# Performance work log

Measured on AMD Instinct MI355X. Metric: run time of the kernel, lower is better.

## Reference

```python
import jax, jax.numpy as jnp
import numpy as np


def setup_inputs() -> dict:
    key = jax.random.key(0)
    B, H, S, D = 4, 16, 2048, 128  # batch, kv heads, seq_len, head_dim
    kv_cache = jax.random.normal(key, (B, H, S, D), dtype=jnp.float32)
    return {"kv_cache": kv_cache, "rank": 64}


def reference(kv_cache, rank):
    # compress(): batched reduced SVD, truncate to `rank` components.
    orig_shape = kv_cache.shape
    S_len, D = orig_shape[-2], orig_shape[-1]
    x = kv_cache.reshape(-1, S_len, D)                 # [N, S, D]
    U, s, Vh = jnp.linalg.svd(x, full_matrices=False)  # U:[N,S,D], s:[N,D], Vh:[N,D,D]
    U_t = U[:, :, :rank]                               # [N, S, r]
    s_t = s[:, :rank]                                  # [N, r]
    Vh_t = Vh[:, :rank, :]                             # [N, r, D]
    left = U_t * s_t[:, None, :]                       # [N, S, r]  (= U * diag(s))
    # decompress(): left @ right^T, right = V[:, :, :rank] so right^T = Vh_t
    reconstructed = jnp.matmul(left, Vh_t)             # [N, S, D]
    return reconstructed.reshape(orig_shape)
```

## Files before the change

kernel.cpp:

```cpp
#include <hip/hip_runtime.h>


#define NM 64
#define SEQ 2048
#define DD 128
#define RR 64
#define NSWEEP 6
#define NROUND (NSWEEP * 64)

#define OFF_VFULL (4194304ULL)
#define OFF_NORM  (8388608ULL)
#define OFF_VT    (33554432ULL)

__device__ __forceinline__ float dot4(float4 a, float4 b) {
  return a.x * b.x + a.y * b.y + a.z * b.z + a.w * b.w;
}

template <int CTRL>
__device__ __forceinline__ float dpp_add(float x) {
  int y = __builtin_amdgcn_update_dpp(0, __float_as_int(x), CTRL, 0xf, 0xf, true);
  return x + __int_as_float(y);
}
__device__ __forceinline__ float red8(float x) {
  x = dpp_add<0xB1>(x);
  x = dpp_add<0x4E>(x);
  x = dpp_add<0x141>(x);
  return x;
}

__device__ __forceinline__ void jrot(float app, float apq, float aqq,
                                     float& c, float& s, float& tv) {
  bool ok = apq * apq > 1e-9f * app * aqq;
  float ap = ok ? apq : 1.f;
  float tau = (aqq - app) / (2.f * ap);
  float t = 1.f / (fabsf(tau) + sqrtf(1.f + tau * tau));
  t = tau < 0.f ? -t : t;
  float cc = 1.f / sqrtf(1.f + t * t);
  float ss = t * cc;
  c = ok ? cc : 1.f;
  s = ok ? ss : 0.f;
  tv = ok ? t : 0.f;
}

__device__ __forceinline__ void rot4(float c, float s, float4 p, float4 q,
                                     float4& np, float4& nq) {
  np.x = c * p.x - s * q.x;  nq.x = s * p.x + c * q.x;
  np.y = c * p.y - s * q.y;  nq.y = s * p.y + c * q.y;
  np.z = c * p.z - s * q.z;  nq.z = s * p.z + c * q.z;
  np.w = c * p.w - s * q.w;  nq.w = s * p.w + c * q.w;
}

__global__ __launch_bounds__(256) void gram_k(const float* __restrict__ X,
                                              float* __restrict__ G) {
  const int m = blockIdx.y;
  const int r0 = blockIdx.x * 32;
  const int tid = threadIdx.x;
  __shared__ __align__(16) float Xs[64][128];
  const float* Xm = X + (size_t)m * SEQ * DD;
  const int ti = tid >> 5;
  const int tj = tid & 31;
  float acc[4][4];
#pragma unroll
  for (int a = 0; a < 4; ++a)
#pragma unroll
    for (int b = 0; b < 4; ++b) acc[a][b] = 0.f;

  for (int s0 = 0; s0 < SEQ; s0 += 64) {
    __syncthreads();
    for (int t = tid; t < 2048; t += 256) {
      int s = t >> 5, c4 = t & 31;
      *(float4*)&Xs[s][c4 * 4] =
          *(const float4*)&Xm[(size_t)(s0 + s) * DD + c4 * 4];
    }
    __syncthreads();
#pragma unroll 4
    for (int s = 0; s < 64; ++s) {
      float4 av = *(const float4*)&Xs[s][r0 + 4 * ti];
      float4 bv = *(const float4*)&Xs[s][4 * tj];
      acc[0][0] += av.x * bv.x; acc[0][1] += av.x * bv.y;
      acc[0][2] += av.x * bv.z; acc[0][3] += av.x * bv.w;
      acc[1][0] += av.y * bv.x; acc[1][1] += av.y * bv.y;
      acc[1][2] += av.y * bv.z; acc[1][3] += av.y * bv.w;
      acc[2][0] += av.z * bv.x; acc[2][1] += av.z * bv.y;
      acc[2][2] += av.z * bv.z; acc[2][3] += av.z * bv.w;
      acc[3][0] += av.w * bv.x; acc[3][1] += av.w * bv.y;
      acc[3][2] += av.w * bv.z; acc[3][3] += av.w * bv.w;
    }
  }
  float* Gm = G + (size_t)m * DD * DD;
#pragma unroll
  for (int a = 0; a < 4; ++a) {
    float4 v = make_float4(acc[a][0], acc[a][1], acc[a][2], acc[a][3]);
    *(float4*)&Gm[(size_t)(r0 + 4 * ti + a) * DD + 4 * tj] = v;
  }
}

__global__ __launch_bounds__(512) void jacobi_nc_k(const float* __restrict__ G,
                                                   float* __restrict__ Vfull,
                                                   float* __restrict__ normg) {
  const int m = blockIdx.x;
  const int tid = threadIdx.x;
  const int g = tid >> 3;
  const int l = tid & 7;
  __shared__ __align__(16) float4 xch[RR * 32];
  __shared__ float nrm[RR];

  const float4* Gm4 = (const float4*)(G + (size_t)m * DD * DD);
  float4 ce[4], co[4];
#pragma unroll
  for (int j = 0; j < 4; ++j) {
    ce[j] = Gm4[(size_t)(2 * g) * 32 + l + 8 * j];
    co[j] = Gm4[(size_t)(2 * g + 1) * 32 + l + 8 * j];
  }
  float nce = 0.f, nco = 0.f;
#pragma unroll
  for (int j = 0; j < 4; ++j) {
    nce += dot4(ce[j], ce[j]);
    nco += dot4(co[j], co[j]);
  }
  nce = red8(nce);
  nco = red8(nco);

  const bool hasR = (g < 63);
  const bool hasL = (g > 0);
  float4* hE = &xch[g * 32];
  float4* hR = &xch[(g + 1) * 32];

  for (int round = 0; round < NROUND; ++round) {
    {
      float apq = 0.f;
#pragma unroll
      for (int j = 0; j < 4; ++j) apq += dot4(ce[j], co[j]);
      apq = red8(apq);
      float c, s, tv;
      jrot(nce, apq, nco, c, s, tv);
#pragma unroll
      for (int j = 0; j < 4; ++j) {
        float4 np, nq;
        rot4(c, s, ce[j], co[j], np, nq);
        ce[j] = nq; co[j] = np;
      }
      float t = nce;
      nce = nco + tv * apq;
      nco = t - tv * apq;
    }
    if (hasL) {
#pragma unroll
      for (int j = 0; j < 4; ++j) hE[l + 8 * j] = ce[j];
      if (l == 0) nrm[g] = nce;
    }
    __syncthreads();
    if (hasR) {
      float4 r4[4];
#pragma unroll
      for (int j = 0; j < 4; ++j) r4[j] = hR[l + 8 * j];
      float nr = nrm[g + 1];
      float apq = 0.f;
#pragma unroll
      for (int j = 0; j < 4; ++j) apq += dot4(co[j], r4[j]);
      apq = red8(apq);
      float c, s, tv;
      jrot(nco, apq, nr, c, s, tv);
#pragma unroll
      for (int j = 0; j < 4; ++j) {
        float4 np, nq;
        rot4(c, s, co[j], r4[j], np, nq);
        hR[l + 8 * j] = np;
        co[j] = nq;
      }
      if (l == 0) nrm[g + 1] = nco - tv * apq;
      nco = nr + tv * apq;
    }
    __syncthreads();
    if (hasL) {
#pragma unroll
      for (int j = 0; j < 4; ++j) ce[j] = hE[l + 8 * j];
      nce = nrm[g];
    }
  }

  float ne = 0.f, no_ = 0.f;
#pragma unroll
  for (int j = 0; j < 4; ++j) {
    ne += dot4(ce[j], ce[j]);
    no_ += dot4(co[j], co[j]);
  }
  ne = red8(ne);
  no_ = red8(no_);
  float4* Ve = (float4*)(Vfull + ((size_t)m * DD + 2 * g) * DD);
  float4* Vo = (float4*)(Vfull + ((size_t)m * DD + 2 * g + 1) * DD);
#pragma unroll
  for (int j = 0; j < 4; ++j) {
    Ve[l + 8 * j] = ce[j];
    Vo[l + 8 * j] = co[j];
  }
  if (l == 0) {
    normg[m * DD + 2 * g] = ne;
    normg[m * DD + 2 * g + 1] = no_;
  }
}

__global__ __launch_bounds__(128) void select_k(const float* __restrict__ Vfull,
                                                const float* __restrict__ normg,
                                                float* __restrict__ Vt) {
  const int m = blockIdx.x;
  const int t = threadIdx.x;
  __shared__ float n[DD];
  __shared__ int inv[RR];
  __shared__ float scl[RR];
  n[t] = normg[m * DD + t];
  __syncthreads();
  float nt = n[t];
  int rk = 0;
  for (int k = 0; k < DD; ++k) {
    float nk = n[k];
    rk += ((nk > nt) || (nk == nt && k < t)) ? 1 : 0;
  }
  if (rk < RR) { inv[rk] = t; scl[rk] = 1.f / sqrtf(nt); }
  __syncthreads();
  for (int r = 0; r < RR; ++r) {
    Vt[((size_t)m * RR + r) * DD + t] =
        Vfull[((size_t)m * DD + inv[r]) * DD + t] * scl[r];
  }
}

__global__ __launch_bounds__(256) void gemm1_k(const float* __restrict__ X,
                                               const float* __restrict__ Vt,
                                               float* __restrict__ W) {
  const int m = blockIdx.y;
  const int s0 = blockIdx.x * 32;
  const int tid = threadIdx.x;
  __shared__ __align__(16) float VtT[128 * 68];
  __shared__ __align__(16) float Xs[32 * 132];
  const float* Vm = Vt + (size_t)m * RR * DD;
  for (int t = tid; t < RR * DD; t += 256) {
    int r = t >> 7, c = t & 127;
    VtT[c * 68 + r] = Vm[t];
  }
  const float* Xm = X + ((size_t)m * SEQ + s0) * DD;
  for (int t = tid; t < 1024; t += 256) {
    int s = t >> 5, c4 = t & 31;
    *(float4*)&Xs[s * 132 + 4 * c4] = *(const float4*)&Xm[(size_t)s * DD + 4 * c4];
  }
  __syncthreads();
  const int ti = tid >> 4;
  const int tj = tid & 15;
  float acc[2][4] = {{0.f, 0.f, 0.f, 0.f}, {0.f, 0.f, 0.f, 0.f}};
#pragma unroll 4
  for (int k = 0; k < DD; ++k) {
    float a0 = Xs[(2 * ti) * 132 + k];
    float a1 = Xs[(2 * ti + 1) * 132 + k];
    float4 bv = *(float4*)&VtT[k * 68 + 4 * tj];
    acc[0][0] += a0 * bv.x; acc[0][1] += a0 * bv.y;
    acc[0][2] += a0 * bv.z; acc[0][3] += a0 * bv.w;
    acc[1][0] += a1 * bv.x; acc[1][1] += a1 * bv.y;
    acc[1][2] += a1 * bv.z; acc[1][3] += a1 * bv.w;
  }
  float* Wm = W + ((size_t)m * SEQ + s0) * RR;
#pragma unroll
  for (int d = 0; d < 2; ++d) {
    float4 v = make_float4(acc[d][0], acc[d][1], acc[d][2], acc[d][3]);
    *(float4*)&Wm[(size_t)(2 * ti + d) * RR + 4 * tj] = v;
  }
}

__global__ __launch_bounds__(256) void gemm2_k(const float* __restrict__ W,
                                               const float* __restrict__ Vt,
                                               float* __restrict__ out) {
  const int m = blockIdx.y;
  const int s0 = blockIdx.x * 32;
  const int tid = threadIdx.x;
  __shared__ __align__(16) float Vts[64 * 132];
  __shared__ __align__(16) float Ws[32 * 68];
  const float* Vm = Vt + (size_t)m * RR * DD;
  for (int t = tid; t < 2048; t += 256) {
    int r = t >> 5, c4 = t & 31;
    *(float4*)&Vts[r * 132 + 4 * c4] = *(const float4*)&Vm[(size_t)r * DD + 4 * c4];
  }
  const float* Wm = W + ((size_t)m * SEQ + s0) * RR;
  for (int t = tid; t < 512; t += 256) {
    int s = t >> 4, c4 = t & 15;
    *(float4*)&Ws[s * 68 + 4 * c4] = *(const float4*)&Wm[(size_t)s * RR + 4 * c4];
  }
  __syncthreads();
  const int ti = tid >> 5;
  const int tj = tid & 31;
  float acc[4][4] = {{0.f,0.f,0.f,0.f},{0.f,0.f,0.f,0.f},
                     {0.f,0.f,0.f,0.f},{0.f,0.f,0.f,0.f}};
#pragma unroll 4
  for (int k = 0; k < RR; ++k) {
    float4 bv = *(float4*)&Vts[k * 132 + 4 * tj];
    float a0 = Ws[(4 * ti + 0) * 68 + k];
    float a1 = Ws[(4 * ti + 1) * 68 + k];
    float a2 = Ws[(4 * ti + 2) * 68 + k];
    float a3 = Ws[(4 * ti + 3) * 68 + k];
    acc[0][0] += a0 * bv.x; acc[0][1] += a0 * bv.y;
    acc[0][2] += a0 * bv.z; acc[0][3] += a0 * bv.w;
    acc[1][0] += a1 * bv.x; acc[1][1] += a1 * bv.y;
    acc[1][2] += a1 * bv.z; acc[1][3] += a1 * bv.w;
    acc[2][0] += a2 * bv.x; acc[2][1] += a2 * bv.y;
    acc[2][2] += a2 * bv.z; acc[2][3] += a2 * bv.w;
    acc[3][0] += a3 * bv.x; acc[3][1] += a3 * bv.y;
    acc[3][2] += a3 * bv.z; acc[3][3] += a3 * bv.w;
  }
  float* Om = out + ((size_t)m * SEQ + s0) * DD;
#pragma unroll
  for (int d = 0; d < 4; ++d) {
    float4 v = make_float4(acc[d][0], acc[d][1], acc[d][2], acc[d][3]);
    *(float4*)&Om[(size_t)(4 * ti + d) * DD + 4 * tj] = v;
  }
}

extern "C" void kernel_launch(void* const* d_in, const int* in_sizes, int n_in,
                              void* d_out, int out_size, void* d_ws, size_t ws_size,
                              hipStream_t stream) {
  (void)in_sizes; (void)n_in; (void)out_size; (void)ws_size;
  const float* X = (const float*)d_in[0];
  float* out = (float*)d_out;
  char* ws = (char*)d_ws;
  float* G = (float*)ws;
  float* Vfull = (float*)(ws + OFF_VFULL);
  float* normg = (float*)(ws + OFF_NORM);
  float* Vt = (float*)(ws + OFF_VT);
  float* W = (float*)ws;

  gram_k<<<dim3(4, NM), 256, 0, stream>>>(X, G);
  jacobi_nc_k<<<NM, 512, 0, stream>>>(G, Vfull, normg);
  select_k<<<NM, 128, 0, stream>>>(Vfull, normg, Vt);
  gemm1_k<<<dim3(SEQ / 32, NM), 256, 0, stream>>>(X, Vt, W);
  gemm2_k<<<dim3(SEQ / 32, NM), 256, 0, stream>>>(W, Vt, out);
}
```

Baseline: 909.5 us.

## Restructure Jacobi kernel to four columns per 16-lane group with double-buffered exchange

The one-sided Jacobi kernel now has each 16-lane group hold four columns instead of two. This halves the number of groups and the per-column work per lane. The exchange now goes through a double-buffered shared array, which cuts each round from two barriers to one. Norms are recomputed at the end of every sweep, and the sweep count rises from 6 to 7, which adds rotation work in exchange for accuracy.

```diff
diff --git a/kernel.cpp b/kernel.cpp
--- a/kernel.cpp
+++ b/kernel.cpp
@@ -5,8 +5,7 @@
 #define SEQ 2048
 #define DD 128
 #define RR 64
-#define NSWEEP 6
-#define NROUND (NSWEEP * 64)
+#define NSWEEP 7
 
 #define OFF_VFULL (4194304ULL)
 #define OFF_NORM  (8388608ULL)
@@ -21,10 +20,11 @@
   int y = __builtin_amdgcn_update_dpp(0, __float_as_int(x), CTRL, 0xf, 0xf, true);
   return x + __int_as_float(y);
 }
-__device__ __forceinline__ float red8(float x) {
+__device__ __forceinline__ float red16(float x) {
   x = dpp_add<0xB1>(x);
   x = dpp_add<0x4E>(x);
   x = dpp_add<0x141>(x);
+  x = dpp_add<0x140>(x);
   return x;
 }
 
@@ -48,6 +48,27 @@
   np.y = c * p.y - s * q.y;  nq.y = s * p.y + c * q.y;
   np.z = c * p.z - s * q.z;  nq.z = s * p.z + c * q.z;
   np.w = c * p.w - s * q.w;  nq.w = s * p.w + c * q.w;
+}
+__device__ __forceinline__ float4 np4(float c, float s, float4 p, float4 q) {
+  return make_float4(c * p.x - s * q.x, c * p.y - s * q.y,
+                     c * p.z - s * q.z, c * p.w - s * q.w);
+}
+__device__ __forceinline__ float4 nq4(float c, float s, float4 p, float4 q) {
+  return make_float4(s * p.x + c * q.x, s * p.y + c * q.y,
+                     s * p.z + c * q.z, s * p.w + c * q.w);
+}
+
+__device__ __forceinline__ void rot2pair(float4* P, float4* Q,
+                                         float& npn, float& nqn) {
+  float apq = red16(dot4(P[0], Q[0]) + dot4(P[1], Q[1]));
+  float c, s, tv;
+  jrot(npn, apq, nqn, c, s, tv);
+  float4 a, b;
+  rot4(c, s, P[0], Q[0], a, b); P[0] = b; Q[0] = a;
+  rot4(c, s, P[1], Q[1], a, b); P[1] = b; Q[1] = a;
+  float t = npn;
+  npn = nqn + tv * apq;
+  nqn = t - tv * apq;
 }
 
 __global__ __launch_bounds__(256) void gram_k(const float* __restrict__ X,
@@ -95,108 +116,102 @@
   }
 }
 
-__global__ __launch_bounds__(512) void jacobi_nc_k(const float* __restrict__ G,
-                                                   float* __restrict__ Vfull,
-                                                   float* __restrict__ normg) {
+__global__ __launch_bounds__(512) void jacobi1b_k(const float* __restrict__ G,
+                                                  float* __restrict__ Vfull,
+                                                  float* __restrict__ normg) {
   const int m = blockIdx.x;
   const int tid = threadIdx.x;
-  const int g = tid >> 3;
-  const int l = tid & 7;
-  __shared__ __align__(16) float4 xch[RR * 32];
-  __shared__ float nrm[RR];
+  const int g = tid >> 4;
+  const int l = tid & 15;
+  __shared__ __align__(16) float4 xch[2][2][32][32];
 
   const float4* Gm4 = (const float4*)(G + (size_t)m * DD * DD);
-  float4 ce[4], co[4];
-#pragma unroll
-  for (int j = 0; j < 4; ++j) {
-    ce[j] = Gm4[(size_t)(2 * g) * 32 + l + 8 * j];
-    co[j] = Gm4[(size_t)(2 * g + 1) * 32 + l + 8 * j];
-  }
-  float nce = 0.f, nco = 0.f;
-#pragma unroll
-  for (int j = 0; j < 4; ++j) {
-    nce += dot4(ce[j], ce[j]);
-    nco += dot4(co[j], co[j]);
-  }
-  nce = red8(nce);
-  nco = red8(nco);
-
-  const bool hasR = (g < 63);
+  float4 c0[2], c1[2], c2[2], c3[2];
+#pragma unroll
+  for (int j = 0; j < 2; ++j) {
+    c0[j] = Gm4[(size_t)(4 * g + 0) * 32 + l + 16 * j];
+    c1[j] = Gm4[(size_t)(4 * g + 1) * 32 + l + 16 * j];
+    c2[j] = Gm4[(size_t)(4 * g + 2) * 32 + l + 16 * j];
+    c3[j] = Gm4[(size_t)(4 * g + 3) * 32 + l + 16 * j];
+  }
+  float n0 = red16(dot4(c0[0], c0[0]) + dot4(c0[1], c0[1]));
+  float n1 = red16(dot4(c1[0], c1[0]) + dot4(c1[1], c1[1]));
+  float n2 = red16(dot4(c2[0], c2[0]) + dot4(c2[1], c2[1]));
+  float n3 = red16(dot4(c3[0], c3[0]) + dot4(c3[1], c3[1]));
+
+  const bool hasR = (g < 31);
   const bool hasL = (g > 0);
-  float4* hE = &xch[g * 32];
-  float4* hR = &xch[(g + 1) * 32];
-
-  for (int round = 0; round < NROUND; ++round) {
-    {
-      float apq = 0.f;
-#pragma unroll
-      for (int j = 0; j < 4; ++j) apq += dot4(ce[j], co[j]);
-      apq = red8(apq);
-      float c, s, tv;
-      jrot(nce, apq, nco, c, s, tv);
-#pragma unroll
-      for (int j = 0; j < 4; ++j) {
-        float4 np, nq;
-        rot4(c, s, ce[j], co[j], np, nq);
-        ce[j] = nq; co[j] = np;
-      }
-      float t = nce;
-      nce = nco + tv * apq;
-      nco = t - tv * apq;
+
+  for (int sweep = 0; sweep < NSWEEP; ++sweep) {
+#pragma unroll 1
+    for (int round = 0; round < 64; ++round) {
+      const int b = round & 1;
+      float* nb = (float*)&xch[b][0][0][0];
+      rot2pair(c0, c1, n0, n1);
+      rot2pair(c2, c3, n2, n3);
+      if (hasL) {
+        xch[b][0][g][l] = c0[0];
+        xch[b][0][g][l + 16] = c0[1];
+        if (l == 0) nb[g] = n0;
+      }
+      if (hasR) {
+        xch[b][1][g][l] = c3[0];
+        xch[b][1][g][l + 16] = c3[1];
+        if (l == 0) nb[64 + g] = n3;
+      }
+      __syncthreads();
+      float4 rq0, rq1, lp0, lp1;
+      float nrq = 0.f, nlp = 0.f;
+      if (hasR) {
+        rq0 = xch[b][0][g + 1][l];
+        rq1 = xch[b][0][g + 1][l + 16];
+        nrq = nb[g + 1];
+      }
+      if (hasL) {
+        lp0 = xch[b][1][g - 1][l];
+        lp1 = xch[b][1][g - 1][l + 16];
+        nlp = nb[64 + g - 1];
+      }
+      rot2pair(c1, c2, n1, n2);
+      if (hasR) {
+        float apq = red16(dot4(c3[0], rq0) + dot4(c3[1], rq1));
+        float c, s, tv;
+        jrot(n3, apq, nrq, c, s, tv);
+        c3[0] = nq4(c, s, c3[0], rq0);
+        c3[1] = nq4(c, s, c3[1], rq1);
+        n3 = nrq + tv * apq;
+      }
+      if (hasL) {
+        float apq = red16(dot4(lp0, c0[0]) + dot4(lp1, c0[1]));
+        float c, s, tv;
+        jrot(nlp, apq, n0, c, s, tv);
+        c0[0] = np4(c, s, lp0, c0[0]);
+        c0[1] = np4(c, s, lp1, c0[1]);
+        n0 = nlp - tv * apq;
+      }
     }
-    if (hasL) {
-#pragma unroll
-      for (int j = 0; j < 4; ++j) hE[l + 8 * j] = ce[j];
-      if (l == 0) nrm[g] = nce;
-    }
-    __syncthreads();
-    if (hasR) {
-      float4 r4[4];
-#pragma unroll
-      for (int j = 0; j < 4; ++j) r4[j] = hR[l + 8 * j];
-      float nr = nrm[g + 1];
-      float apq = 0.f;
-#pragma unroll
-      for (int j = 0; j < 4; ++j) apq += dot4(co[j], r4[j]);
-      apq = red8(apq);
-      float c, s, tv;
-      jrot(nco, apq, nr, c, s, tv);
-#pragma unroll
-      for (int j = 0; j < 4; ++j) {
-        float4 np, nq;
-        rot4(c, s, co[j], r4[j], np, nq);
-        hR[l + 8 * j] = np;
-        co[j] = nq;
-      }
-      if (l == 0) nrm[g + 1] = nco - tv * apq;
-      nco = nr + tv * apq;
-    }
-    __syncthreads();
-    if (hasL) {
-#pragma unroll
-      for (int j = 0; j < 4; ++j) ce[j] = hE[l + 8 * j];
-      nce = nrm[g];
-    }
-  }
-
-  float ne = 0.f, no_ = 0.f;
-#pragma unroll
-  for (int j = 0; j < 4; ++j) {
-    ne += dot4(ce[j], ce[j]);
-    no_ += dot4(co[j], co[j]);
-  }
-  ne = red8(ne);
-  no_ = red8(no_);
-  float4* Ve = (float4*)(Vfull + ((size_t)m * DD + 2 * g) * DD);
-  float4* Vo = (float4*)(Vfull + ((size_t)m * DD + 2 * g + 1) * DD);
-#pragma unroll
-  for (int j = 0; j < 4; ++j) {
-    Ve[l + 8 * j] = ce[j];
-    Vo[l + 8 * j] = co[j];
+    n0 = red16(dot4(c0[0], c0[0]) + dot4(c0[1], c0[1]));
+    n1 = red16(dot4(c1[0], c1[0]) + dot4(c1[1], c1[1]));
+    n2 = red16(dot4(c2[0], c2[0]) + dot4(c2[1], c2[1]));
+    n3 = red16(dot4(c3[0], c3[0]) + dot4(c3[1], c3[1]));
+  }
+
+  float4* V0 = (float4*)(Vfull + ((size_t)m * DD + 4 * g + 0) * DD);
+  float4* V1 = (float4*)(Vfull + ((size_t)m * DD + 4 * g + 1) * DD);
+  float4* V2 = (float4*)(Vfull + ((size_t)m * DD + 4 * g + 2) * DD);
+  float4* V3 = (float4*)(Vfull + ((size_t)m * DD + 4 * g + 3) * DD);
+#pragma unroll
+  for (int j = 0; j < 2; ++j) {
+    V0[l + 16 * j] = c0[j];
+    V1[l + 16 * j] = c1[j];
+    V2[l + 16 * j] = c2[j];
+    V3[l + 16 * j] = c3[j];
   }
   if (l == 0) {
-    normg[m * DD + 2 * g] = ne;
-    normg[m * DD + 2 * g + 1] = no_;
+    normg[m * DD + 4 * g + 0] = n0;
+    normg[m * DD + 4 * g + 1] = n1;
+    normg[m * DD + 4 * g + 2] = n2;
+    normg[m * DD + 4 * g + 3] = n3;
   }
 }
 
@@ -325,7 +340,7 @@
   float* W = (float*)ws;
 
   gram_k<<<dim3(4, NM), 256, 0, stream>>>(X, G);
-  jacobi_nc_k<<<NM, 512, 0, stream>>>(G, Vfull, normg);
+  jacobi1b_k<<<NM, 512, 0, stream>>>(G, Vfull, normg);
   select_k<<<NM, 128, 0, stream>>>(Vfull, normg, Vt);
   gemm1_k<<<dim3(SEQ / 32, NM), 256, 0, stream>>>(X, Vt, W);
   gemm2_k<<<dim3(SEQ / 32, NM), 256, 0, stream>>>(W, Vt, out);
```

Result: slower. 1.375 ms (+51.2%).
